# Kernel tuning notes

Measured on AMD Instinct MI355X. Metric: run time of the kernel, lower is better.

## Reference

```python
import jax, jax.numpy as jnp
import numpy as np

B, S, E, H = 8, 2048, 512, 8
DH = E // H
NEG = -1e30


def setup_inputs() -> dict:
    key = jax.random.key(0)
    ks = jax.random.split(key, 6)
    return {
        "x": jax.random.normal(ks[0], (B, S, E), dtype=jnp.float32),
        "W_qkv": jax.random.normal(ks[1], (E, 3 * E), dtype=jnp.float32) * 0.02,
        "b_qkv": jax.random.normal(ks[2], (3 * E,), dtype=jnp.float32) * 0.02,
        "W_out": jax.random.normal(ks[3], (E, E), dtype=jnp.float32) * 0.02,
        "b_out": jax.random.normal(ks[4], (E,), dtype=jnp.float32) * 0.02,
        "rel_pos": jax.random.normal(ks[5], (1, H, S, S), dtype=jnp.float32) * 0.02,
    }


def reference(x, W_qkv, b_qkv, W_out, b_out, rel_pos):
    b, s, e = x.shape
    scale = DH ** -0.5
    qkv = x @ W_qkv + b_qkv                     # [b, s, 3e]
    qkv = qkv.reshape(b, s, 3, H, DH)
    q = jnp.transpose(qkv[:, :, 0], (0, 2, 1, 3))  # [b, h, s, dh]
    k = jnp.transpose(qkv[:, :, 1], (0, 2, 1, 3))
    v = jnp.transpose(qkv[:, :, 2], (0, 2, 1, 3))
    scores = jnp.einsum("bhqd,bhkd->bhqk", q, k) * scale
    scores = scores + rel_pos[:, :, :s, :s]
    causal = jnp.tril(jnp.ones((s, s), dtype=bool))
    scores = jnp.where(causal[None, None], scores, NEG)
    attn = jax.nn.softmax(scores, axis=-1)
    out = jnp.einsum("bhqk,bhkd->bhqd", attn, v)  # [b, h, s, dh]
    out = jnp.transpose(out, (0, 2, 1, 3)).reshape(b, s, e)
    return out @ W_out + b_out
```

## Files before the change

kernel.cpp:

```cpp
#include <hip/hip_runtime.h>
#include <cstdint>


#define DEVI __device__ __forceinline__

typedef __bf16 bf8 __attribute__((ext_vector_type(8)));
typedef float f4 __attribute__((ext_vector_type(4)));
typedef unsigned short us8 __attribute__((ext_vector_type(8)));
typedef unsigned short us4 __attribute__((ext_vector_type(4)));

typedef const unsigned int __attribute__((address_space(1))) gu32;
typedef unsigned int __attribute__((address_space(3))) lu32;

DEVI unsigned short f2bf(float f) {
  unsigned u = __builtin_bit_cast(unsigned, f);
  u += 0x7fffu + ((u >> 16) & 1u);
  return (unsigned short)(u >> 16);
}

DEVI unsigned short cbf(float f) {
  return __builtin_bit_cast(unsigned short, (__bf16)f);
}

DEVI void gl_lds16(const void* g, void* l) {
  __builtin_amdgcn_global_load_lds((gu32*)g, (lu32*)l, 16, 0, 0);
}

__global__ __launch_bounds__(256) void k_convert_x(const float* __restrict__ x,
                                                   unsigned short* __restrict__ xb) {
  int c = blockIdx.x * 256 + threadIdx.x;
  int row = c >> 6, cl = c & 63;
  const float* s = x + ((size_t)row << 9) + (cl << 3);
  float4 a = *(const float4*)s;
  float4 b = *(const float4*)(s + 4);
  us8 o;
  o[0]=f2bf(a.x); o[1]=f2bf(a.y); o[2]=f2bf(a.z); o[3]=f2bf(a.w);
  o[4]=f2bf(b.x); o[5]=f2bf(b.y); o[6]=f2bf(b.z); o[7]=f2bf(b.w);
  int p = (cl & ~7) | ((cl & 7) ^ (row & 7));
  *(us8*)(xb + ((size_t)row << 9) + (p << 3)) = o;
}

__global__ __launch_bounds__(256) void k_transpose_w(const float* __restrict__ W,
                                                     unsigned short* __restrict__ Wt, int N) {
  __shared__ float t[32][33];
  int k0 = blockIdx.x * 32, n0 = blockIdx.y * 32;
  int tx = threadIdx.x & 31, ty = threadIdx.x >> 5;
#pragma unroll
  for (int r = 0; r < 4; ++r)
    t[ty + r * 8][tx] = W[(size_t)(k0 + ty + r * 8) * N + n0 + tx];
  __syncthreads();
#pragma unroll
  for (int r = 0; r < 4; ++r) {
    int n = n0 + ty + r * 8, k = k0 + tx;
    int k2 = (k & ~63) | ((((k >> 3) & 7) ^ (n & 7)) << 3) | (k & 7);
    Wt[((size_t)n << 9) + k2] = f2bf(t[tx][ty + r * 8]);
  }
}

__global__ __launch_bounds__(256) void k_relconv(const float* __restrict__ rel,
                                                 unsigned short* __restrict__ relt) {
  int t = blockIdx.x * 256 + threadIdx.x;
  int lane = t & 63, ct = (t >> 6) & 3, kt = (t >> 8) & 31, q16 = (t >> 13) & 127, h = t >> 20;
  if (kt > (q16 >> 2)) return;
  int row = (q16 << 4) + (lane & 15);
  int col = (kt << 6) + (ct << 4) + ((lane >> 4) << 2);
  float4 v = *(const float4*)(rel + ((size_t)h << 22) + ((size_t)row << 11) + col);
  us4 o;
  o[0] = f2bf(v.x); o[1] = f2bf(v.y); o[2] = f2bf(v.z); o[3] = f2bf(v.w);
  size_t idx = ((((((size_t)h << 7) | q16) << 5) | kt) << 2 | ct) << 6 | lane;
  *(us4*)(relt + (idx << 2)) = o;
}

template <int EPI>
__global__ __launch_bounds__(256, 2)
void k_gemm(const unsigned short* __restrict__ Ag, const unsigned short* __restrict__ Bg,
            const float* __restrict__ bias, float* __restrict__ Of,
            unsigned short* __restrict__ Oq, unsigned short* __restrict__ Ok,
            unsigned short* __restrict__ Ov) {
  __shared__ __align__(16) unsigned short lds[128 * 64 * 2];
  unsigned short* Al = lds;
  unsigned short* Bl = lds + 128 * 64;
  const int tid = threadIdx.x, wv = tid >> 6, lane = tid & 63, g = lane >> 4, cl = lane & 15;
  const int wm = wv >> 1, wn = wv & 1;
  const int row0 = blockIdx.x * 128, col0 = blockIdx.y * 128;
  f4 acc[4][4];
#pragma unroll
  for (int i = 0; i < 4; ++i)
#pragma unroll
    for (int j = 0; j < 4; ++j) acc[i][j] = (f4){0.f, 0.f, 0.f, 0.f};

  for (int kt = 0; kt < 8; ++kt) {
#pragma unroll
    for (int j = 0; j < 4; ++j) {
      int ci = wv * 4 + j;
      int gci = ci * 64 + lane;
      int r = gci >> 3, cc = gci & 7;
      gl_lds16(Ag + ((size_t)(row0 + r) << 9) + kt * 64 + cc * 8, Al + ci * 512);
      gl_lds16(Bg + ((size_t)(col0 + r) << 9) + kt * 64 + cc * 8, Bl + ci * 512);
    }
    __syncthreads();
#pragma unroll
    for (int kk = 0; kk < 2; ++kk) {
      bf8 af[4], bb[4];
#pragma unroll
      for (int mf = 0; mf < 4; ++mf) {
        int r = wm * 64 + mf * 16 + cl;
        int cc = (kk * 4 + g) ^ (r & 7);
        af[mf] = *(const bf8*)(Al + r * 64 + cc * 8);
      }
#pragma unroll
      for (int nf = 0; nf < 4; ++nf) {
        int r = wn * 64 + nf * 16 + cl;
        int cc = (kk * 4 + g) ^ (r & 7);
        bb[nf] = *(const bf8*)(Bl + r * 64 + cc * 8);
      }
#pragma unroll
      for (int mf = 0; mf < 4; ++mf)
#pragma unroll
        for (int nf = 0; nf < 4; ++nf)
          acc[mf][nf] = __builtin_amdgcn_mfma_f32_16x16x32_bf16(af[mf], bb[nf], acc[mf][nf], 0, 0, 0);
    }
    __syncthreads();
  }

  if (EPI == 1) {
#pragma unroll
    for (int nf = 0; nf < 4; ++nf) {
      int col = col0 + wn * 64 + nf * 16 + cl;
      float bv = bias[col];
#pragma unroll
      for (int mf = 0; mf < 4; ++mf) {
#pragma unroll
        for (int j = 0; j < 4; ++j) {
          int row = row0 + wm * 64 + mf * 16 + 4 * g + j;
          Of[((size_t)row << 9) + col] = acc[mf][nf][j] + bv;
        }
      }
    }
  } else {
    const int which = col0 >> 9;
#pragma unroll
    for (int nf = 0; nf < 4; ++nf) {
      int col = col0 + wn * 64 + nf * 16 + cl;
      float bv = bias[col];
      int d = col & 63, h = (col >> 6) & 7;
#pragma unroll
      for (int mf = 0; mf < 4; ++mf) {
        int row = row0 + wm * 64 + mf * 16 + 4 * g;
        int b = row >> 11, s = row & 2047;
        size_t fb = ((size_t)b * 8 + h) * 131072;
        if (which == 0) {
#pragma unroll
          for (int j = 0; j < 4; ++j) {
            int ss = s + j;
            size_t off = fb + (size_t)((ss >> 4) * 1024 + (d >> 5) * 512 +
                                       (((d >> 3) & 3) * 16 + (ss & 15)) * 8 + (d & 7));
            Oq[off] = f2bf((acc[mf][nf][j] + bv) * 0.125f);
          }
        } else if (which == 1) {
#pragma unroll
          for (int j = 0; j < 4; ++j) {
            int ss = s + j;
            size_t off = fb + (size_t)((ss >> 6) * 4096 + (d >> 5) * 2048 + ((ss >> 4) & 3) * 512 +
                                       (((d >> 3) & 3) * 16 + (ss & 15)) * 8 + (d & 7));
            Ok[off] = f2bf(acc[mf][nf][j] + bv);
          }
        } else {
          us4 o;
#pragma unroll
          for (int j = 0; j < 4; ++j) o[j] = f2bf(acc[mf][nf][j] + bv);
          size_t off = fb + (size_t)((s >> 6) * 4096 + ((s >> 5) & 1) * 2048 + (d >> 4) * 512 +
                                     ((((s >> 3) & 3) * 16) + (d & 15)) * 8 + (s & 7));
          *(us4*)(Ov + off) = o;
        }
      }
    }
  }
}

template <bool RELT>
__global__ __launch_bounds__(256, 4)
void k_attn(const unsigned short* __restrict__ Qf, const unsigned short* __restrict__ Kf,
            const unsigned short* __restrict__ Vf, const float* __restrict__ rel,
            const unsigned short* __restrict__ relt, unsigned short* __restrict__ AO) {
  __shared__ __align__(16) unsigned short Pl[4][16 * 72];
  const int tid = threadIdx.x, wv = tid >> 6, lane = tid & 63, g = lane >> 4, cl = lane & 15;
  int bid = blockIdx.x;
  int h = bid & 7;
  int rest = bid >> 3;
  int q16 = 127 - (rest >> 1);
  int b = ((rest & 1) << 2) | wv;
  const int rX = q16 << 4;
  const int ktop = q16 >> 2;
  const int qrow = rX + cl;
  size_t fb = (((size_t)b << 3) + h) * 131072;
  const unsigned short* Qp = Qf + fb;
  const unsigned short* Kp = Kf + fb;
  const unsigned short* Vp = Vf + fb;
  const float* relp = rel + ((size_t)h << 22);
  unsigned short* pw = Pl[wv];

  bf8 qf[2];
#pragma unroll
  for (int kk = 0; kk < 2; ++kk)
    qf[kk] = *(const bf8*)(Qp + q16 * 1024 + kk * 512 + lane * 8);

  f4 ot[4];
  float mr = -1e30f, lr = 0.f;
#pragma unroll
  for (int ct = 0; ct < 4; ++ct) ot[ct] = (f4){0.f, 0.f, 0.f, 0.f};

  for (int kt = 0; kt <= ktop; ++kt) {
    const int kb = kt << 6;
    const unsigned short* Kt = Kp + kt * 4096;
    const unsigned short* Vt = Vp + kt * 4096;
    bf8 kf[2][4], vf[2][4];
#pragma unroll
    for (int kk = 0; kk < 2; ++kk)
#pragma unroll
      for (int ct = 0; ct < 4; ++ct)
        kf[kk][ct] = *(const bf8*)(Kt + kk * 2048 + ct * 512 + lane * 8);
#pragma unroll
    for (int kk = 0; kk < 2; ++kk)
#pragma unroll
      for (int ct = 0; ct < 4; ++ct)
        vf[kk][ct] = *(const bf8*)(Vt + kk * 2048 + ct * 512 + lane * 8);
    us4 rt4[4];
    float4 rl4[4];
    if constexpr (RELT) {
      const unsigned short* tb = relt + (((((size_t)h << 7) | q16) << 5) | kt) * 1024;
#pragma unroll
      for (int ct = 0; ct < 4; ++ct)
        rt4[ct] = *(const us4*)(tb + ((ct << 6) | lane) * 4);
    } else {
#pragma unroll
      for (int ct = 0; ct < 4; ++ct)
        rl4[ct] = *(const float4*)(relp + ((size_t)qrow << 11) + kb + ct * 16 + g * 4);
    }
    f4 st[4];
#pragma unroll
    for (int ct = 0; ct < 4; ++ct) st[ct] = (f4){0.f, 0.f, 0.f, 0.f};
#pragma unroll
    for (int kk = 0; kk < 2; ++kk)
#pragma unroll
      for (int ct = 0; ct < 4; ++ct)
        st[ct] = __builtin_amdgcn_mfma_f32_16x16x32_bf16(kf[kk][ct], qf[kk], st[ct], 0, 0, 0);
    if constexpr (RELT) {
#pragma unroll
      for (int ct = 0; ct < 4; ++ct)
#pragma unroll
        for (int j = 0; j < 4; ++j)
          st[ct][j] += __builtin_bit_cast(float, (unsigned)rt4[ct][j] << 16);
    } else {
#pragma unroll
      for (int ct = 0; ct < 4; ++ct) {
        st[ct][0] += rl4[ct].x; st[ct][1] += rl4[ct].y;
        st[ct][2] += rl4[ct].z; st[ct][3] += rl4[ct].w;
      }
    }
    if (kt == ktop) {
#pragma unroll
      for (int ct = 0; ct < 4; ++ct) {
        int kc0 = kb + ct * 16 + 4 * g;
#pragma unroll
        for (int j = 0; j < 4; ++j)
          if (kc0 + j > qrow) st[ct][j] = -1e30f;
      }
    }
    float m0 = fmaxf(fmaxf(st[0][0], st[0][1]), fmaxf(st[0][2], st[0][3]));
#pragma unroll
    for (int ct = 1; ct < 4; ++ct)
      m0 = fmaxf(m0, fmaxf(fmaxf(st[ct][0], st[ct][1]), fmaxf(st[ct][2], st[ct][3])));
    m0 = fmaxf(m0, __shfl_xor(m0, 16));
    m0 = fmaxf(m0, __shfl_xor(m0, 32));
    float mn = fmaxf(mr, m0);
    float al = __expf(mr - mn);
    mr = mn;
#pragma unroll
    for (int ct = 0; ct < 4; ++ct)
#pragma unroll
      for (int j = 0; j < 4; ++j) st[ct][j] = __expf(st[ct][j] - mn);
    float rs = 0.f;
#pragma unroll
    for (int ct = 0; ct < 4; ++ct)
      rs += (st[ct][0] + st[ct][1]) + (st[ct][2] + st[ct][3]);
    rs += __shfl_xor(rs, 16);
    rs += __shfl_xor(rs, 32);
    lr = lr * al + rs;
#pragma unroll
    for (int ct = 0; ct < 4; ++ct) {
      ot[ct][0] *= al; ot[ct][1] *= al; ot[ct][2] *= al; ot[ct][3] *= al;
    }
#pragma unroll
    for (int ct = 0; ct < 4; ++ct) {
      us4 pk;
      pk[0] = cbf(st[ct][0]); pk[1] = cbf(st[ct][1]);
      pk[2] = cbf(st[ct][2]); pk[3] = cbf(st[ct][3]);
      *(us4*)(pw + cl * 72 + ct * 16 + g * 4) = pk;
    }
#pragma unroll
    for (int kk = 0; kk < 2; ++kk) {
      bf8 pf = __builtin_bit_cast(bf8, *(const us8*)(pw + cl * 72 + kk * 32 + g * 8));
#pragma unroll
      for (int ct = 0; ct < 4; ++ct)
        ot[ct] = __builtin_amdgcn_mfma_f32_16x16x32_bf16(vf[kk][ct], pf, ot[ct], 0, 0, 0);
    }
  }
  float inv = 1.0f / lr;
  const int s = qrow;
  unsigned short* aor = AO + (((size_t)b << 11) + s) * 512 + h * 64;
#pragma unroll
  for (int ct = 0; ct < 4; ++ct) {
    int chunk = 2 * ct + (g >> 1);
    int base = (4 * (g & 1)) | ((chunk ^ (s & 7)) << 3);
    us4 o;
    o[0] = cbf(ot[ct][0] * inv); o[1] = cbf(ot[ct][1] * inv);
    o[2] = cbf(ot[ct][2] * inv); o[3] = cbf(ot[ct][3] * inv);
    *(us4*)(aor + base) = o;
  }
}

extern "C" void kernel_launch(void* const* d_in, const int* in_sizes, int n_in,
                              void* d_out, int out_size, void* d_ws, size_t ws_size,
                              hipStream_t stream) {
  const float* x    = (const float*)d_in[0];
  const float* Wqkv = (const float*)d_in[1];
  const float* bqkv = (const float*)d_in[2];
  const float* Wout = (const float*)d_in[3];
  const float* bout = (const float*)d_in[4];
  const float* rel  = (const float*)d_in[5];
  float* out = (float*)d_out;

  unsigned short* Qw  = (unsigned short*)d_ws;
  unsigned short* Kw  = Qw  + 8388608;
  unsigned short* Vw  = Kw  + 8388608;
  unsigned short* XA  = Vw  + 8388608;
  unsigned short* WtQ = XA  + 8388608;
  unsigned short* WtO = WtQ + 786432;
  unsigned short* relt= WtO + 262144;
  const bool useT = ws_size >= (34603008ULL + 33554432ULL) * 2ULL;

  k_convert_x<<<dim3(4096), dim3(256), 0, stream>>>(x, XA);
  k_transpose_w<<<dim3(16, 48), dim3(256), 0, stream>>>(Wqkv, WtQ, 1536);
  k_transpose_w<<<dim3(16, 16), dim3(256), 0, stream>>>(Wout, WtO, 512);
  if (useT) k_relconv<<<dim3(32768), dim3(256), 0, stream>>>(rel, relt);
  k_gemm<0><<<dim3(128, 12), dim3(256), 0, stream>>>(XA, WtQ, bqkv, nullptr, Qw, Kw, Vw);
  if (useT) k_attn<true ><<<dim3(2048), dim3(256), 0, stream>>>(Qw, Kw, Vw, rel, relt, XA);
  else      k_attn<false><<<dim3(2048), dim3(256), 0, stream>>>(Qw, Kw, Vw, rel, relt, XA);
  k_gemm<1><<<dim3(128, 4), dim3(256), 0, stream>>>(XA, WtO, bout, out, nullptr, nullptr, nullptr);
}
```

Measured before the change: 200.3 us.

## Double-buffer K/V/rel tile loads in attention and switch softmax to exp2

Restructures the attention key-tile loop into a ping-pong pattern that issues the next tile's K, V and rel-pos register loads before computing the current tile, so global-load latency is hidden behind MFMA and softmax work. It also folds log2(e) into the Q scaling and the rel-pos conversion so the softmax can use exp2f instead of __expf. The cost is roughly double the live register footprint for K/V fragments, which under launch_bounds(256,4) risks spills or lower occupancy.

```diff
diff --git a/kernel.cpp b/kernel.cpp
--- a/kernel.cpp
+++ b/kernel.cpp
@@ -11,6 +11,8 @@
 
 typedef const unsigned int __attribute__((address_space(1))) gu32;
 typedef unsigned int __attribute__((address_space(3))) lu32;
+
+#define L2E 1.44269504088896f
 
 DEVI unsigned short f2bf(float f) {
   unsigned u = __builtin_bit_cast(unsigned, f);
@@ -66,7 +68,8 @@
   int col = (kt << 6) + (ct << 4) + ((lane >> 4) << 2);
   float4 v = *(const float4*)(rel + ((size_t)h << 22) + ((size_t)row << 11) + col);
   us4 o;
-  o[0] = f2bf(v.x); o[1] = f2bf(v.y); o[2] = f2bf(v.z); o[3] = f2bf(v.w);
+  o[0] = f2bf(v.x * L2E); o[1] = f2bf(v.y * L2E);
+  o[2] = f2bf(v.z * L2E); o[3] = f2bf(v.w * L2E);
   size_t idx = ((((((size_t)h << 7) | q16) << 5) | kt) << 2 | ct) << 6 | lane;
   *(us4*)(relt + (idx << 2)) = o;
 }
@@ -155,7 +158,7 @@
             int ss = s + j;
             size_t off = fb + (size_t)((ss >> 4) * 1024 + (d >> 5) * 512 +
                                        (((d >> 3) & 3) * 16 + (ss & 15)) * 8 + (d & 7));
-            Oq[off] = f2bf((acc[mf][nf][j] + bv) * 0.125f);
+            Oq[off] = f2bf((acc[mf][nf][j] + bv) * (0.125f * L2E));
           }
         } else if (which == 1) {
 #pragma unroll
@@ -177,6 +180,94 @@
     }
   }
 }
+
+
+#define LOADT(KF, VF, RT, RL, KT)                                             \
+  do {                                                                        \
+    const unsigned short* Kt_ = Kp + (KT) * 4096;                             \
+    const unsigned short* Vt_ = Vp + (KT) * 4096;                             \
+    _Pragma("unroll") for (int kk = 0; kk < 2; ++kk)                          \
+      _Pragma("unroll") for (int ct = 0; ct < 4; ++ct)                        \
+        KF[kk][ct] = *(const bf8*)(Kt_ + kk * 2048 + ct * 512 + lane * 8);    \
+    _Pragma("unroll") for (int kk = 0; kk < 2; ++kk)                          \
+      _Pragma("unroll") for (int ct = 0; ct < 4; ++ct)                        \
+        VF[kk][ct] = *(const bf8*)(Vt_ + kk * 2048 + ct * 512 + lane * 8);    \
+    if constexpr (RELT) {                                                     \
+      const unsigned short* tb_ =                                             \
+          relt + (((((size_t)h << 7) | q16) << 5) | (KT)) * 1024;             \
+      _Pragma("unroll") for (int ct = 0; ct < 4; ++ct)                        \
+        RT[ct] = *(const us4*)(tb_ + ((ct << 6) | lane) * 4);                 \
+    } else {                                                                  \
+      _Pragma("unroll") for (int ct = 0; ct < 4; ++ct)                        \
+        RL[ct] = *(const float4*)(relp + ((size_t)qrow << 11) + ((KT) << 6) + \
+                                  ct * 16 + g * 4);                           \
+    }                                                                         \
+  } while (0)
+
+#define COMPT(KF, VF, RT, RL, KT)                                             \
+  do {                                                                        \
+    const int kb_ = (KT) << 6;                                                \
+    f4 st[4];                                                                 \
+    _Pragma("unroll") for (int ct = 0; ct < 4; ++ct)                          \
+      st[ct] = (f4){0.f, 0.f, 0.f, 0.f};                                      \
+    _Pragma("unroll") for (int kk = 0; kk < 2; ++kk)                          \
+      _Pragma("unroll") for (int ct = 0; ct < 4; ++ct)                        \
+        st[ct] = __builtin_amdgcn_mfma_f32_16x16x32_bf16(KF[kk][ct], qf[kk],  \
+                                                         st[ct], 0, 0, 0);    \
+    if constexpr (RELT) {                                                     \
+      _Pragma("unroll") for (int ct = 0; ct < 4; ++ct)                        \
+        _Pragma("unroll") for (int j = 0; j < 4; ++j)                         \
+          st[ct][j] += __builtin_bit_cast(float, (unsigned)RT[ct][j] << 16);  \
+    } else {                                                                  \
+      _Pragma("unroll") for (int ct = 0; ct < 4; ++ct) {                      \
+        st[ct][0] = fmaf(RL[ct].x, L2E, st[ct][0]);                           \
+        st[ct][1] = fmaf(RL[ct].y, L2E, st[ct][1]);                           \
+        st[ct][2] = fmaf(RL[ct].z, L2E, st[ct][2]);                           \
+        st[ct][3] = fmaf(RL[ct].w, L2E, st[ct][3]);                           \
+      }                                                                       \
+    }                                                                         \
+    if ((KT) == ktop) {                                                       \
+      _Pragma("unroll") for (int ct = 0; ct < 4; ++ct) {                      \
+        int kc0_ = kb_ + ct * 16 + 4 * g;                                     \
+        _Pragma("unroll") for (int j = 0; j < 4; ++j)                         \
+          if (kc0_ + j > qrow) st[ct][j] = -1e30f;                            \
+      }                                                                       \
+    }                                                                         \
+    float m0_ = fmaxf(fmaxf(st[0][0], st[0][1]), fmaxf(st[0][2], st[0][3]));  \
+    _Pragma("unroll") for (int ct = 1; ct < 4; ++ct)                          \
+      m0_ = fmaxf(m0_, fmaxf(fmaxf(st[ct][0], st[ct][1]),                     \
+                             fmaxf(st[ct][2], st[ct][3])));                   \
+    m0_ = fmaxf(m0_, __shfl_xor(m0_, 16));                                    \
+    m0_ = fmaxf(m0_, __shfl_xor(m0_, 32));                                    \
+    float mn_ = fmaxf(mr, m0_);                                               \
+    float al_ = exp2f(mr - mn_);                                              \
+    mr = mn_;                                                                 \
+    _Pragma("unroll") for (int ct = 0; ct < 4; ++ct)                          \
+      _Pragma("unroll") for (int j = 0; j < 4; ++j)                           \
+        st[ct][j] = exp2f(st[ct][j] - mn_);                                   \
+    float rs_ = 0.f;                                                          \
+    _Pragma("unroll") for (int ct = 0; ct < 4; ++ct)                          \
+      rs_ += (st[ct][0] + st[ct][1]) + (st[ct][2] + st[ct][3]);               \
+    rs_ += __shfl_xor(rs_, 16);                                               \
+    rs_ += __shfl_xor(rs_, 32);                                               \
+    lr = lr * al_ + rs_;                                                      \
+    _Pragma("unroll") for (int ct = 0; ct < 4; ++ct) {                        \
+      ot[ct][0] *= al_; ot[ct][1] *= al_; ot[ct][2] *= al_; ot[ct][3] *= al_; \
+    }                                                                         \
+    _Pragma("unroll") for (int ct = 0; ct < 4; ++ct) {                        \
+      us4 pk_;                                                                \
+      pk_[0] = cbf(st[ct][0]); pk_[1] = cbf(st[ct][1]);                       \
+      pk_[2] = cbf(st[ct][2]); pk_[3] = cbf(st[ct][3]);                       \
+      *(us4*)(pw + cl * 72 + ct * 16 + g * 4) = pk_;                          \
+    }                                                                         \
+    _Pragma("unroll") for (int kk = 0; kk < 2; ++kk) {                        \
+      bf8 pf_ = __builtin_bit_cast(bf8,                                       \
+                  *(const us8*)(pw + cl * 72 + kk * 32 + g * 8));             \
+      _Pragma("unroll") for (int ct = 0; ct < 4; ++ct)                        \
+        ot[ct] = __builtin_amdgcn_mfma_f32_16x16x32_bf16(VF[kk][ct], pf_,     \
+                                                         ot[ct], 0, 0, 0);    \
+    }                                                                         \
+  } while (0)
 
 template <bool RELT>
 __global__ __launch_bounds__(256, 4)
@@ -210,102 +301,20 @@
 #pragma unroll
   for (int ct = 0; ct < 4; ++ct) ot[ct] = (f4){0.f, 0.f, 0.f, 0.f};
 
-  for (int kt = 0; kt <= ktop; ++kt) {
-    const int kb = kt << 6;
-    const unsigned short* Kt = Kp + kt * 4096;
-    const unsigned short* Vt = Vp + kt * 4096;
-    bf8 kf[2][4], vf[2][4];
-#pragma unroll
-    for (int kk = 0; kk < 2; ++kk)
-#pragma unroll
-      for (int ct = 0; ct < 4; ++ct)
-        kf[kk][ct] = *(const bf8*)(Kt + kk * 2048 + ct * 512 + lane * 8);
-#pragma unroll
-    for (int kk = 0; kk < 2; ++kk)
-#pragma unroll
-      for (int ct = 0; ct < 4; ++ct)
-        vf[kk][ct] = *(const bf8*)(Vt + kk * 2048 + ct * 512 + lane * 8);
-    us4 rt4[4];
-    float4 rl4[4];
-    if constexpr (RELT) {
-      const unsigned short* tb = relt + (((((size_t)h << 7) | q16) << 5) | kt) * 1024;
-#pragma unroll
-      for (int ct = 0; ct < 4; ++ct)
-        rt4[ct] = *(const us4*)(tb + ((ct << 6) | lane) * 4);
-    } else {
-#pragma unroll
-      for (int ct = 0; ct < 4; ++ct)
-        rl4[ct] = *(const float4*)(relp + ((size_t)qrow << 11) + kb + ct * 16 + g * 4);
-    }
-    f4 st[4];
-#pragma unroll
-    for (int ct = 0; ct < 4; ++ct) st[ct] = (f4){0.f, 0.f, 0.f, 0.f};
-#pragma unroll
-    for (int kk = 0; kk < 2; ++kk)
-#pragma unroll
-      for (int ct = 0; ct < 4; ++ct)
-        st[ct] = __builtin_amdgcn_mfma_f32_16x16x32_bf16(kf[kk][ct], qf[kk], st[ct], 0, 0, 0);
-    if constexpr (RELT) {
-#pragma unroll
-      for (int ct = 0; ct < 4; ++ct)
-#pragma unroll
-        for (int j = 0; j < 4; ++j)
-          st[ct][j] += __builtin_bit_cast(float, (unsigned)rt4[ct][j] << 16);
-    } else {
-#pragma unroll
-      for (int ct = 0; ct < 4; ++ct) {
-        st[ct][0] += rl4[ct].x; st[ct][1] += rl4[ct].y;
-        st[ct][2] += rl4[ct].z; st[ct][3] += rl4[ct].w;
-      }
-    }
-    if (kt == ktop) {
-#pragma unroll
-      for (int ct = 0; ct < 4; ++ct) {
-        int kc0 = kb + ct * 16 + 4 * g;
-#pragma unroll
-        for (int j = 0; j < 4; ++j)
-          if (kc0 + j > qrow) st[ct][j] = -1e30f;
-      }
-    }
-    float m0 = fmaxf(fmaxf(st[0][0], st[0][1]), fmaxf(st[0][2], st[0][3]));
-#pragma unroll
-    for (int ct = 1; ct < 4; ++ct)
-      m0 = fmaxf(m0, fmaxf(fmaxf(st[ct][0], st[ct][1]), fmaxf(st[ct][2], st[ct][3])));
-    m0 = fmaxf(m0, __shfl_xor(m0, 16));
-    m0 = fmaxf(m0, __shfl_xor(m0, 32));
-    float mn = fmaxf(mr, m0);
-    float al = __expf(mr - mn);
-    mr = mn;
-#pragma unroll
-    for (int ct = 0; ct < 4; ++ct)
-#pragma unroll
-      for (int j = 0; j < 4; ++j) st[ct][j] = __expf(st[ct][j] - mn);
-    float rs = 0.f;
-#pragma unroll
-    for (int ct = 0; ct < 4; ++ct)
-      rs += (st[ct][0] + st[ct][1]) + (st[ct][2] + st[ct][3]);
-    rs += __shfl_xor(rs, 16);
-    rs += __shfl_xor(rs, 32);
-    lr = lr * al + rs;
-#pragma unroll
-    for (int ct = 0; ct < 4; ++ct) {
-      ot[ct][0] *= al; ot[ct][1] *= al; ot[ct][2] *= al; ot[ct][3] *= al;
-    }
-#pragma unroll
-    for (int ct = 0; ct < 4; ++ct) {
-      us4 pk;
-      pk[0] = cbf(st[ct][0]); pk[1] = cbf(st[ct][1]);
-      pk[2] = cbf(st[ct][2]); pk[3] = cbf(st[ct][3]);
-      *(us4*)(pw + cl * 72 + ct * 16 + g * 4) = pk;
-    }
-#pragma unroll
-    for (int kk = 0; kk < 2; ++kk) {
-      bf8 pf = __builtin_bit_cast(bf8, *(const us8*)(pw + cl * 72 + kk * 32 + g * 8));
-#pragma unroll
-      for (int ct = 0; ct < 4; ++ct)
-        ot[ct] = __builtin_amdgcn_mfma_f32_16x16x32_bf16(vf[kk][ct], pf, ot[ct], 0, 0, 0);
-    }
-  }
+  bf8 kfA[2][4], vfA[2][4], kfB[2][4], vfB[2][4];
+  us4 rtA[4], rtB[4];
+  float4 rlA[4], rlB[4];
+  LOADT(kfA, vfA, rtA, rlA, 0);
+  int kt = 0;
+  for (;;) {
+    if (kt + 1 <= ktop) LOADT(kfB, vfB, rtB, rlB, kt + 1);
+    COMPT(kfA, vfA, rtA, rlA, kt);
+    if (++kt > ktop) break;
+    if (kt + 1 <= ktop) LOADT(kfA, vfA, rtA, rlA, kt + 1);
+    COMPT(kfB, vfB, rtB, rlB, kt);
+    if (++kt > ktop) break;
+  }
+
   float inv = 1.0f / lr;
   const int s = qrow;
   unsigned short* aor = AO + (((size_t)b << 11) + s) * 512 + h * 64;
```

After: 626.8 us. 213% more time.

## Prefetch next K tile, fold log2e into Q/rel, add MFMA priority hints

Applied to the files above, without the earlier changes.

K fragments for the next key tile are loaded right after the current QK MFMAs so global load latency overlaps the softmax and PV work. log2(e) is folded into the Q scale and the relative-position bias, so the softmax can use exp2 directly instead of exp. s_setprio raises wave priority around the MFMA blocks. This adds register pressure from the extra live K fragments, and bf16 rounding of the rel bias now happens after scaling.

```diff
diff --git a/kernel.cpp b/kernel.cpp
--- a/kernel.cpp
+++ b/kernel.cpp
@@ -11,6 +11,8 @@
 
 typedef const unsigned int __attribute__((address_space(1))) gu32;
 typedef unsigned int __attribute__((address_space(3))) lu32;
+
+#define L2E 1.44269504088896f
 
 DEVI unsigned short f2bf(float f) {
   unsigned u = __builtin_bit_cast(unsigned, f);
@@ -66,7 +68,8 @@
   int col = (kt << 6) + (ct << 4) + ((lane >> 4) << 2);
   float4 v = *(const float4*)(rel + ((size_t)h << 22) + ((size_t)row << 11) + col);
   us4 o;
-  o[0] = f2bf(v.x); o[1] = f2bf(v.y); o[2] = f2bf(v.z); o[3] = f2bf(v.w);
+  o[0] = f2bf(v.x * L2E); o[1] = f2bf(v.y * L2E);
+  o[2] = f2bf(v.z * L2E); o[3] = f2bf(v.w * L2E);
   size_t idx = ((((((size_t)h << 7) | q16) << 5) | kt) << 2 | ct) << 6 | lane;
   *(us4*)(relt + (idx << 2)) = o;
 }
@@ -155,7 +158,7 @@
             int ss = s + j;
             size_t off = fb + (size_t)((ss >> 4) * 1024 + (d >> 5) * 512 +
                                        (((d >> 3) & 3) * 16 + (ss & 15)) * 8 + (d & 7));
-            Oq[off] = f2bf((acc[mf][nf][j] + bv) * 0.125f);
+            Oq[off] = f2bf((acc[mf][nf][j] + bv) * (0.125f * L2E));
           }
         } else if (which == 1) {
 #pragma unroll
@@ -210,16 +213,17 @@
 #pragma unroll
   for (int ct = 0; ct < 4; ++ct) ot[ct] = (f4){0.f, 0.f, 0.f, 0.f};
 
+  bf8 kf[2][4];
+#pragma unroll
+  for (int kk = 0; kk < 2; ++kk)
+#pragma unroll
+    for (int ct = 0; ct < 4; ++ct)
+      kf[kk][ct] = *(const bf8*)(Kp + kk * 2048 + ct * 512 + lane * 8);
+
   for (int kt = 0; kt <= ktop; ++kt) {
     const int kb = kt << 6;
-    const unsigned short* Kt = Kp + kt * 4096;
     const unsigned short* Vt = Vp + kt * 4096;
-    bf8 kf[2][4], vf[2][4];
-#pragma unroll
-    for (int kk = 0; kk < 2; ++kk)
-#pragma unroll
-      for (int ct = 0; ct < 4; ++ct)
-        kf[kk][ct] = *(const bf8*)(Kt + kk * 2048 + ct * 512 + lane * 8);
+    bf8 vf[2][4];
 #pragma unroll
     for (int kk = 0; kk < 2; ++kk)
 #pragma unroll
@@ -240,11 +244,21 @@
     f4 st[4];
 #pragma unroll
     for (int ct = 0; ct < 4; ++ct) st[ct] = (f4){0.f, 0.f, 0.f, 0.f};
+    __builtin_amdgcn_s_setprio(1);
 #pragma unroll
     for (int kk = 0; kk < 2; ++kk)
 #pragma unroll
       for (int ct = 0; ct < 4; ++ct)
         st[ct] = __builtin_amdgcn_mfma_f32_16x16x32_bf16(kf[kk][ct], qf[kk], st[ct], 0, 0, 0);
+    __builtin_amdgcn_s_setprio(0);
+    if (kt < ktop) {
+      const unsigned short* Kn = Kp + (kt + 1) * 4096;
+#pragma unroll
+      for (int kk = 0; kk < 2; ++kk)
+#pragma unroll
+        for (int ct = 0; ct < 4; ++ct)
+          kf[kk][ct] = *(const bf8*)(Kn + kk * 2048 + ct * 512 + lane * 8);
+    }
     if constexpr (RELT) {
 #pragma unroll
       for (int ct = 0; ct < 4; ++ct)
@@ -254,8 +268,10 @@
     } else {
 #pragma unroll
       for (int ct = 0; ct < 4; ++ct) {
-        st[ct][0] += rl4[ct].x; st[ct][1] += rl4[ct].y;
-        st[ct][2] += rl4[ct].z; st[ct][3] += rl4[ct].w;
+        st[ct][0] = fmaf(rl4[ct].x, L2E, st[ct][0]);
+        st[ct][1] = fmaf(rl4[ct].y, L2E, st[ct][1]);
+        st[ct][2] = fmaf(rl4[ct].z, L2E, st[ct][2]);
+        st[ct][3] = fmaf(rl4[ct].w, L2E, st[ct][3]);
       }
     }
     if (kt == ktop) {
@@ -274,12 +290,12 @@
     m0 = fmaxf(m0, __shfl_xor(m0, 16));
     m0 = fmaxf(m0, __shfl_xor(m0, 32));
     float mn = fmaxf(mr, m0);
-    float al = __expf(mr - mn);
+    float al = exp2f(mr - mn);
     mr = mn;
 #pragma unroll
     for (int ct = 0; ct < 4; ++ct)
 #pragma unroll
-      for (int j = 0; j < 4; ++j) st[ct][j] = __expf(st[ct][j] - mn);
+      for (int j = 0; j < 4; ++j) st[ct][j] = exp2f(st[ct][j] - mn);
     float rs = 0.f;
 #pragma unroll
     for (int ct = 0; ct < 4; ++ct)
@@ -298,6 +314,7 @@
       pk[2] = cbf(st[ct][2]); pk[3] = cbf(st[ct][3]);
       *(us4*)(pw + cl * 72 + ct * 16 + g * 4) = pk;
     }
+    __builtin_amdgcn_s_setprio(1);
 #pragma unroll
     for (int kk = 0; kk < 2; ++kk) {
       bf8 pf = __builtin_bit_cast(bf8, *(const us8*)(pw + cl * 72 + kk * 32 + g * 8));
@@ -305,6 +322,7 @@
       for (int ct = 0; ct < 4; ++ct)
         ot[ct] = __builtin_amdgcn_mfma_f32_16x16x32_bf16(vf[kk][ct], pf, ot[ct], 0, 0, 0);
     }
+    __builtin_amdgcn_s_setprio(0);
   }
   float inv = 1.0f / lr;
   const int s = qrow;
```

New measurement: 214.8 us. +7.2%, slower.
